# Kernel optimization log

Hardware: AMD Instinct MI355X
Metric: run time of the kernel (lower is better)

Reference implementation:

```python
import jax, jax.numpy as jnp
import numpy as np

B, S, D_MODEL = 4, 4096, 1024
H, KD, F = 16, 64, 256
KERNEL_SCALE = 1.0
NORM = 1.0 / np.sqrt(KD).astype(np.float32)  # 1/sqrt(key_dim)
EPS = 1e-6


def setup_inputs() -> dict:
    key = jax.random.key(0)
    ks = jax.random.split(key, 12)
    s = 0.02
    x = jax.random.normal(ks[0], (B, S, D_MODEL), dtype=jnp.float32)
    Wq = jax.random.normal(ks[1], (D_MODEL, H * KD), dtype=jnp.float32) * s
    bq = jnp.zeros((H * KD,), jnp.float32)
    Wk = jax.random.normal(ks[2], (D_MODEL, H * KD), dtype=jnp.float32) * s
    bk = jnp.zeros((H * KD,), jnp.float32)
    Wv = jax.random.normal(ks[3], (D_MODEL, H * KD), dtype=jnp.float32) * s
    bv = jnp.zeros((H * KD,), jnp.float32)
    # RFF params (non-trainable in original; orthogonal-ish random here)
    rff_W = jax.random.normal(ks[4], (KD, F), dtype=jnp.float32)
    q_, _ = jnp.linalg.qr(rff_W.T)  # (F, KD) -> orthonormal rows subset
    rff_W = q_.T[:KD, :F].astype(jnp.float32)
    rff_b = jax.random.uniform(ks[5], (F,), jnp.float32, 0.0, 2.0 * np.pi)
    Wo = jax.random.normal(ks[6], (H * KD, D_MODEL), dtype=jnp.float32) * s
    bo = jnp.zeros((D_MODEL,), jnp.float32)
    return {"x": x, "Wq": Wq, "bq": bq, "Wk": Wk, "bk": bk, "Wv": Wv,
            "bv": bv, "rff_W": rff_W, "rff_b": rff_b, "Wo": Wo, "bo": bo}


def _split_heads(t):
    # [B, S, H*KD] -> [B, H, S, KD]
    return t.reshape(B, S, H, KD).transpose(0, 2, 1, 3)


def _rff(t, rff_W, rff_b):
    # RandomFourierFeatures: cos((x*scale) @ W + b) * sqrt(2/F)
    proj = jnp.einsum('bhsd,df->bhsf', t * KERNEL_SCALE, rff_W) + rff_b
    return jnp.cos(proj) * np.sqrt(2.0 / F).astype(np.float32)


def reference(x, Wq, bq, Wk, bk, Wv, bv, rff_W, rff_b, Wo, bo):
    q = _split_heads(x @ Wq + bq)  # [B,H,S,KD]
    k = _split_heads(x @ Wk + bk)
    v = _split_heads(x @ Wv + bv)
    q_prime = _rff(q * NORM, rff_W, rff_b)  # [B,H,S,F]
    k_prime = _rff(k * NORM, rff_W, rff_b)
    # Non-causal FAVOR+ linear attention: O(L)
    kv = jnp.einsum('bhsf,bhsd->bhfd', k_prime, v)          # [B,H,F,KD]
    k_sum = jnp.sum(k_prime, axis=2)                         # [B,H,F]
    num = jnp.einsum('bhsf,bhfd->bhsd', q_prime, kv)         # [B,H,S,KD]
    den = jnp.einsum('bhsf,bhf->bhs', q_prime, k_sum)        # [B,H,S]
    out = num / (den + EPS)[..., None]
    out = out.transpose(0, 2, 1, 3).reshape(B, S, H * KD)    # merge heads
    return out @ Wo + bo
```

## Files before the change

kernel.cpp:

```cpp
#include <hip/hip_runtime.h>
#include <hip/hip_bf16.h>
#include <math.h>

#define B_SZ    4
#define S_LEN   4096
#define DMODEL  1024
#define NH      16
#define KDIM    64
#define NF      256
#define NROWS   (B_SZ * S_LEN)
#define NCHUNK  8
#define RFF_SCALE 0.08838834764831845f
#define NORM_Q    0.125f

typedef __attribute__((ext_vector_type(8))) short s8v;
typedef __attribute__((ext_vector_type(4))) float f4v;

static __device__ __forceinline__ unsigned short f2bf(float f) {
  unsigned u = __float_as_uint(f);
  unsigned r = (u + 0x7FFFu + ((u >> 16) & 1u)) >> 16;
  return (unsigned short)r;
}

#define MFMA16(a, b, c) __builtin_amdgcn_mfma_f32_16x16x32_bf16((a), (b), (c), 0, 0, 0)

__device__ __forceinline__ void glds16(const void* g, void* l) {
  __builtin_amdgcn_global_load_lds(
      (const __attribute__((address_space(1))) void*)g,
      (__attribute__((address_space(3))) void*)l, 16, 0, 0);
}

__global__ __launch_bounds__(256) void cast_bf16_kernel(
    const float* __restrict__ src, unsigned short* __restrict__ dst, int n8)
{
  int i = blockIdx.x * 256 + threadIdx.x;
  if (i >= n8) return;
  const float* s = src + (size_t)i * 8;
  float4 a = *(const float4*)s;
  float4 b = *(const float4*)(s + 4);
  union { s8v v; unsigned short u[8]; } o;
  o.u[0]=f2bf(a.x); o.u[1]=f2bf(a.y); o.u[2]=f2bf(a.z); o.u[3]=f2bf(a.w);
  o.u[4]=f2bf(b.x); o.u[5]=f2bf(b.y); o.u[6]=f2bf(b.z); o.u[7]=f2bf(b.w);
  *(s8v*)(dst + (size_t)i * 8) = o.v;
}

__global__ __launch_bounds__(256) void transpose_cast_kernel(
    const float* __restrict__ W, unsigned short* __restrict__ WT)
{
  __shared__ float t[32][33];
  const int k0 = blockIdx.y * 32, n0 = blockIdx.x * 32;
  const int c = threadIdx.x & 31, r4 = threadIdx.x >> 5;
#pragma unroll
  for (int i = 0; i < 4; ++i) {
    int row = r4 + i * 8;
    t[row][c] = W[(size_t)(k0 + row) * 1024 + n0 + c];
  }
  __syncthreads();
#pragma unroll
  for (int i = 0; i < 4; ++i) {
    int row = r4 + i * 8;
    WT[(size_t)(n0 + row) * 1024 + k0 + c] = f2bf(t[c][row]);
  }
}

__global__ __launch_bounds__(256) void prep_rff_kernel(
    const float* __restrict__ rffW, unsigned short* __restrict__ rffWT)
{
  int i = blockIdx.x * 256 + threadIdx.x;
  int f = i >> 6, d = i & 63;
  rffWT[(size_t)f * 64 + d] = f2bf(rffW[(size_t)d * 256 + f] * NORM_Q);
}

template <int OUT_BF16, int QKV_FUSED>
__global__ __launch_bounds__(512, 2) void gemm_bt_kernel(
    const unsigned short* __restrict__ A,
    const unsigned short* __restrict__ BT0,
    const unsigned short* __restrict__ BT1,
    const unsigned short* __restrict__ BT2,
    const float* __restrict__ bias0, const float* __restrict__ bias1,
    const float* __restrict__ bias2,
    void* __restrict__ out0, void* __restrict__ out1, void* __restrict__ out2,
    int M, int N, int K, int NXT)
{
  __shared__ __align__(16) unsigned short As[2][16384];
  __shared__ __align__(16) unsigned short Bs[2][16384];
  const int tid = threadIdx.x;
  const int lane = tid & 63, wave = tid >> 6;

  int wg = blockIdx.x;
  {
    const int nwg = gridDim.x;
    const int q = nwg >> 3, r = nwg & 7;
    const int xcd = wg & 7, pos = wg >> 3;
    wg = (xcd < r ? xcd * (q + 1) : r * (q + 1) + (xcd - r) * q) + pos;
  }
  const int m0 = (wg / NXT) * 256;
  int ngl = (wg % NXT) * 256;
  const unsigned short* BT = BT0;
  const float* bias = bias0;
  void* outp = out0;
  if (QKV_FUSED) {
    int which = ngl >> 10;
    if (which == 1) { BT = BT1; bias = bias1; outp = out1; }
    else if (which == 2) { BT = BT2; bias = bias2; outp = out2; }
    ngl &= 1023;
  }
  const int n0 = ngl;

  const int trow = tid >> 3;
  const int g8 = (((lane & 7) ^ (trow & 7)) * 8);
  const unsigned short* aPtr = A  + (size_t)(m0 + trow) * K + g8;
  const unsigned short* bPtr = BT + (size_t)(n0 + trow) * K + g8;
  const int NT = K >> 6;

  auto STAGE = [&](int ts, int h) {
    if (ts >= NT) return;
    const int buf = ts & 1, half = h >> 1;
    const size_t go = (size_t)half * 128 * K + (size_t)ts * 64;
    if ((h & 1) == 0) {
      unsigned short* lp = &As[buf][half * 8192 + wave * 512];
      glds16(aPtr + go, lp);
      glds16(aPtr + go + (size_t)64 * K, lp + 4096);
    } else {
      unsigned short* lp = &Bs[buf][half * 8192 + wave * 512];
      glds16(bPtr + go, lp);
      glds16(bPtr + go + (size_t)64 * K, lp + 4096);
    }
  };

  const int col = lane & 15, quad = lane >> 4;
  const int wm = (wave >> 2) * 128;
  const int wn = (wave & 3) * 64;
  const int c7 = col & 7;
  const int idxA0 = (wm + col) * 64 + ((quad ^ c7) * 8);
  const int idxA1 = (wm + col) * 64 + (((4 + quad) ^ c7) * 8);
  const int idxB0 = (wn + col) * 64 + ((quad ^ c7) * 8);
  const int idxB1 = (wn + col) * 64 + (((4 + quad) ^ c7) * 8);

  f4v acc[2][4][4];
  const f4v zz = {0.f, 0.f, 0.f, 0.f};
#pragma unroll
  for (int h = 0; h < 2; ++h)
#pragma unroll
    for (int i = 0; i < 4; ++i)
#pragma unroll
      for (int j = 0; j < 4; ++j) acc[h][i][j] = zz;

  STAGE(0, 0); STAGE(0, 1); STAGE(0, 2); STAGE(0, 3);
  STAGE(1, 0); STAGE(1, 1); STAGE(1, 2);
  asm volatile("s_waitcnt vmcnt(6)" ::: "memory");
  __builtin_amdgcn_s_barrier();

  s8v a0[4][2], a1[4][2], b0[2][2], b1[2][2];
  {
    const unsigned short* pA = As[0];
    const unsigned short* pB = Bs[0];
#pragma unroll
    for (int u = 0; u < 2; ++u) {
      b0[u][0] = *(const s8v*)&pB[idxB0 + u * 1024];
      b0[u][1] = *(const s8v*)&pB[idxB1 + u * 1024];
    }
#pragma unroll
    for (int x = 0; x < 4; ++x) {
      a0[x][0] = *(const s8v*)&pA[idxA0 + x * 1024];
      a0[x][1] = *(const s8v*)&pA[idxA1 + x * 1024];
    }
  }

  for (int t = 0; t < NT; ++t) {
    const int buf = t & 1;
    const unsigned short* pA = As[buf];
    const unsigned short* pB = Bs[buf];
    const unsigned short* qA = As[buf ^ 1];
    const unsigned short* qB = Bs[buf ^ 1];

    __builtin_amdgcn_s_barrier();
    asm volatile("s_waitcnt lgkmcnt(0)" ::: "memory");
    __builtin_amdgcn_sched_barrier(0);
#pragma unroll
    for (int u = 0; u < 2; ++u) {
      b1[u][0] = *(const s8v*)&pB[idxB0 + 2048 + u * 1024];
      b1[u][1] = *(const s8v*)&pB[idxB1 + 2048 + u * 1024];
    }
    __builtin_amdgcn_sched_barrier(0);
#pragma unroll
    for (int x = 0; x < 4; ++x) {
      a1[x][0] = *(const s8v*)&pA[idxA0 + 4096 + x * 1024];
      a1[x][1] = *(const s8v*)&pA[idxA1 + 4096 + x * 1024];
    }
    __builtin_amdgcn_sched_barrier(0);
    __builtin_amdgcn_s_setprio(1);
#pragma unroll
    for (int x = 0; x < 4; ++x)
#pragma unroll
      for (int u = 0; u < 2; ++u) {
        acc[0][x][u] = MFMA16(a0[x][0], b0[u][0], acc[0][x][u]);
        acc[0][x][u] = MFMA16(a0[x][1], b0[u][1], acc[0][x][u]);
      }
    __builtin_amdgcn_s_setprio(0);
    __builtin_amdgcn_sched_barrier(0);

    __builtin_amdgcn_s_barrier();
    STAGE(t + 1, 3);
    asm volatile("s_waitcnt lgkmcnt(8)" ::: "memory");
    __builtin_amdgcn_sched_barrier(0);
    __builtin_amdgcn_s_setprio(1);
#pragma unroll
    for (int x = 0; x < 4; ++x)
#pragma unroll
      for (int u = 0; u < 2; ++u) {
        acc[0][x][2 + u] = MFMA16(a0[x][0], b1[u][0], acc[0][x][2 + u]);
        acc[0][x][2 + u] = MFMA16(a0[x][1], b1[u][1], acc[0][x][2 + u]);
      }
    __builtin_amdgcn_s_setprio(0);
    __builtin_amdgcn_sched_barrier(0);

    __builtin_amdgcn_s_barrier();
    STAGE(t + 2, 1);
    asm volatile("s_waitcnt lgkmcnt(0)" ::: "memory");
    __builtin_amdgcn_sched_barrier(0);
    __builtin_amdgcn_s_setprio(1);
#pragma unroll
    for (int x = 0; x < 4; ++x)
#pragma unroll
      for (int u = 0; u < 2; ++u) {
        acc[1][x][2 + u] = MFMA16(a1[x][0], b1[u][0], acc[1][x][2 + u]);
        acc[1][x][2 + u] = MFMA16(a1[x][1], b1[u][1], acc[1][x][2 + u]);
      }
    __builtin_amdgcn_s_setprio(0);
    __builtin_amdgcn_sched_barrier(0);

    __builtin_amdgcn_s_barrier();
    STAGE(t + 2, 0);
    STAGE(t + 2, 2);
    if (t < NT - 2) asm volatile("s_waitcnt vmcnt(6)" ::: "memory");
    else            asm volatile("s_waitcnt vmcnt(0)" ::: "memory");
    __builtin_amdgcn_sched_barrier(0);
    s8v b0n[2][2], a0n[4][2];
#pragma unroll
    for (int u = 0; u < 2; ++u) {
      b0n[u][0] = *(const s8v*)&qB[idxB0 + u * 1024];
      b0n[u][1] = *(const s8v*)&qB[idxB1 + u * 1024];
    }
    __builtin_amdgcn_sched_barrier(0);
#pragma unroll
    for (int x = 0; x < 4; ++x) {
      a0n[x][0] = *(const s8v*)&qA[idxA0 + x * 1024];
      a0n[x][1] = *(const s8v*)&qA[idxA1 + x * 1024];
    }
    __builtin_amdgcn_sched_barrier(0);
    __builtin_amdgcn_s_setprio(1);
#pragma unroll
    for (int x = 0; x < 4; ++x)
#pragma unroll
      for (int u = 0; u < 2; ++u) {
        acc[1][x][u] = MFMA16(a1[x][0], b0[u][0], acc[1][x][u]);
        acc[1][x][u] = MFMA16(a1[x][1], b0[u][1], acc[1][x][u]);
      }
    __builtin_amdgcn_s_setprio(0);
    __builtin_amdgcn_sched_barrier(0);
#pragma unroll
    for (int u = 0; u < 2; ++u) { b0[u][0] = b0n[u][0]; b0[u][1] = b0n[u][1]; }
#pragma unroll
    for (int x = 0; x < 4; ++x) { a0[x][0] = a0n[x][0]; a0[x][1] = a0n[x][1]; }
  }

#pragma unroll
  for (int h = 0; h < 2; ++h) {
#pragma unroll
    for (int i = 0; i < 4; ++i) {
#pragma unroll
      for (int j = 0; j < 4; ++j) {
        int n = n0 + wn + j * 16 + col;
        float bv = bias[n];
#pragma unroll
        for (int r = 0; r < 4; ++r) {
          int m = m0 + wm + h * 64 + i * 16 + quad * 4 + r;
          float v = acc[h][i][j][r] + bv;
          if (OUT_BF16)
            ((unsigned short*)outp)[(size_t)m * N + n] = f2bf(v);
          else
            ((float*)outp)[(size_t)m * N + n] = v;
        }
      }
    }
  }
}

__global__ __launch_bounds__(256) void kv_kernel(
    const unsigned short* __restrict__ kg, const unsigned short* __restrict__ vg,
    const unsigned short* __restrict__ rffWT, const float* __restrict__ rffb,
    float* __restrict__ pkv)
{
  __shared__ __align__(16) unsigned short vT[80 * 72];
  __shared__ __align__(16) unsigned short kps[256 * 72];
  const int bh = blockIdx.x, chunk = blockIdx.y;
  const int b = bh >> 4, h = bh & 15;
  const int tid = threadIdx.x;
  const int lane = tid & 63, wave = tid >> 6;
  const int col = lane & 15, quad = lane >> 4;
  const f4v zz = {0.f, 0.f, 0.f, 0.f};

  s8v wf[2][4];
  float bfv[4];
#pragma unroll
  for (int ks = 0; ks < 2; ++ks)
#pragma unroll
    for (int t = 0; t < 4; ++t)
      wf[ks][t] = *(const s8v*)(rffWT +
          (size_t)(wave * 64 + t * 16 + col) * 64 + ks * 32 + quad * 8);
#pragma unroll
  for (int j = 0; j < 4; ++j) bfv[j] = rffb[wave * 64 + j * 16 + col];

  for (int e = tid; e < 1024; e += 256) {
    int r = 64 + (e >> 6), s = e & 63;
    vT[r * 72 + s] = (r == 64) ? (unsigned short)0x3F80 : (unsigned short)0;
  }

  f4v kvacc[4][5];
#pragma unroll
  for (int i = 0; i < 4; ++i)
#pragma unroll
    for (int j = 0; j < 5; ++j) kvacc[i][j] = zz;

  const int sA = tid & 63,        chA = tid >> 6;
  const int sB = (tid + 256) & 63, chB = (tid + 256) >> 6;

  union U { s8v v; unsigned short u[8]; };
  U v0, v1;
  s8v kf[2][4];
  {
    const int s0 = chunk * 512;
    v0.v = *(const s8v*)(vg + ((size_t)(b * S_LEN + s0 + sA)) * DMODEL + h * KDIM + chA * 8);
    v1.v = *(const s8v*)(vg + ((size_t)(b * S_LEN + s0 + sB)) * DMODEL + h * KDIM + chB * 8);
#pragma unroll
    for (int ks = 0; ks < 2; ++ks)
#pragma unroll
      for (int t = 0; t < 4; ++t)
        kf[ks][t] = *(const s8v*)(kg +
            ((size_t)(b * S_LEN + s0 + t * 16 + col)) * DMODEL + h * KDIM + ks * 32 + quad * 8);
  }

  for (int st = 0; st < 8; ++st) {
    const int s0 = chunk * 512 + st * 64;
    __syncthreads();
#pragma unroll
    for (int j = 0; j < 8; ++j) vT[(chA * 8 + j) * 72 + sA] = v0.u[j];
#pragma unroll
    for (int j = 0; j < 8; ++j) vT[(chB * 8 + j) * 72 + sB] = v1.u[j];
    f4v p[4][4];
#pragma unroll
    for (int i = 0; i < 4; ++i)
#pragma unroll
      for (int j = 0; j < 4; ++j) p[i][j] = zz;
#pragma unroll
    for (int ks = 0; ks < 2; ++ks)
#pragma unroll
      for (int i = 0; i < 4; ++i)
#pragma unroll
        for (int j = 0; j < 4; ++j) p[i][j] = MFMA16(kf[ks][i], wf[ks][j], p[i][j]);
    U n0, n1;
    s8v kn[2][4];
    if (st < 7) {
      const int s1 = s0 + 64;
      n0.v = *(const s8v*)(vg + ((size_t)(b * S_LEN + s1 + sA)) * DMODEL + h * KDIM + chA * 8);
      n1.v = *(const s8v*)(vg + ((size_t)(b * S_LEN + s1 + sB)) * DMODEL + h * KDIM + chB * 8);
#pragma unroll
      for (int ks = 0; ks < 2; ++ks)
#pragma unroll
        for (int t = 0; t < 4; ++t)
          kn[ks][t] = *(const s8v*)(kg +
              ((size_t)(b * S_LEN + s1 + t * 16 + col)) * DMODEL + h * KDIM + ks * 32 + quad * 8);
    }
#pragma unroll
    for (int j = 0; j < 4; ++j) {
      int f = wave * 64 + j * 16 + col;
#pragma unroll
      for (int i = 0; i < 4; ++i) {
        union { unsigned long long d; unsigned short u[4]; } pk;
#pragma unroll
        for (int r = 0; r < 4; ++r)
          pk.u[r] = f2bf(__cosf(p[i][j][r] + bfv[j]) * RFF_SCALE);
        *(unsigned long long*)&kps[f * 72 + i * 16 + quad * 4] = pk.d;
      }
    }
    __syncthreads();
#pragma unroll
    for (int ks = 0; ks < 2; ++ks) {
      s8v af[4], bf[5];
#pragma unroll
      for (int t = 0; t < 4; ++t)
        af[t] = *(const s8v*)&kps[(wave * 64 + t * 16 + col) * 72 + ks * 32 + quad * 8];
#pragma unroll
      for (int t = 0; t < 5; ++t)
        bf[t] = *(const s8v*)&vT[(t * 16 + col) * 72 + ks * 32 + quad * 8];
#pragma unroll
      for (int i = 0; i < 4; ++i)
#pragma unroll
        for (int j = 0; j < 5; ++j)
          kvacc[i][j] = MFMA16(af[i], bf[j], kvacc[i][j]);
    }
    v0 = n0; v1 = n1;
#pragma unroll
    for (int ks = 0; ks < 2; ++ks)
#pragma unroll
      for (int t = 0; t < 4; ++t) kf[ks][t] = kn[ks][t];
  }
  const size_t base = ((size_t)(chunk * 64 + bh)) * NF * 80;
#pragma unroll
  for (int i = 0; i < 4; ++i)
#pragma unroll
    for (int r = 0; r < 4; ++r) {
      int f = wave * 64 + i * 16 + quad * 4 + r;
#pragma unroll
      for (int j = 0; j < 5; ++j)
        pkv[base + (size_t)f * 80 + j * 16 + col] = kvacc[i][j][r];
    }
}

__global__ __launch_bounds__(256) void reduce_kv_kernel(
    const float* __restrict__ pkv, unsigned short* __restrict__ kvT)
{
  __shared__ unsigned short lt[80 * 64];
  const int bh = blockIdx.x >> 2, qt = blockIdx.x & 3;
  const int f0 = qt * 64;
  for (int e = threadIdx.x; e < 64 * 80; e += 256) {
    int fl = e / 80, d = e - fl * 80;
    float s = 0.f;
#pragma unroll
    for (int c = 0; c < NCHUNK; ++c)
      s += pkv[((size_t)(c * 64 + bh)) * NF * 80 + (size_t)(f0 + fl) * 80 + d];
    lt[d * 64 + fl] = f2bf(s);
  }
  __syncthreads();
  for (int o = threadIdx.x; o < 80 * 64; o += 256) {
    int d = o >> 6, fl = o & 63;
    kvT[(size_t)bh * 80 * NF + d * 256 + f0 + fl] = lt[o];
  }
}

__global__ __launch_bounds__(256) void attn_kernel(
    const unsigned short* __restrict__ qg, const unsigned short* __restrict__ kvTg,
    const unsigned short* __restrict__ rffWT, const float* __restrict__ rffb,
    unsigned short* __restrict__ att)
{
  __shared__ __align__(16) unsigned short qps[64 * 264];
  __shared__ __align__(16) unsigned short kvs[80 * 264];
  const int bh = blockIdx.x;
  const int b = bh >> 4, h = bh & 15;
  const int tid = threadIdx.x;
  const int lane = tid & 63, wave = tid >> 6;
  const int col = lane & 15, quad = lane >> 4;
  const f4v zz = {0.f, 0.f, 0.f, 0.f};

  s8v wf[2][4];
  float bfv[4];
#pragma unroll
  for (int ks = 0; ks < 2; ++ks)
#pragma unroll
    for (int t = 0; t < 4; ++t)
      wf[ks][t] = *(const s8v*)(rffWT +
          (size_t)(wave * 64 + t * 16 + col) * 64 + ks * 32 + quad * 8);
#pragma unroll
  for (int j = 0; j < 4; ++j) bfv[j] = rffb[wave * 64 + j * 16 + col];

  for (int c = tid; c < 2560; c += 256) {
    int d = c >> 5, ch = c & 31;
    *(s8v*)&kvs[d * 264 + ch * 8] =
        *(const s8v*)(kvTg + (size_t)bh * 80 * NF + d * 256 + ch * 8);
  }

  s8v qf[2][4];
  {
    const int s0 = blockIdx.y * 512;
#pragma unroll
    for (int ks = 0; ks < 2; ++ks)
#pragma unroll
      for (int t = 0; t < 4; ++t)
        qf[ks][t] = *(const s8v*)(qg +
            ((size_t)(b * S_LEN + s0 + t * 16 + col)) * DMODEL + h * KDIM + ks * 32 + quad * 8);
  }

  for (int it = 0; it < 8; ++it) {
    const int s0 = blockIdx.y * 512 + it * 64;
    f4v p[4][4];
#pragma unroll
    for (int i = 0; i < 4; ++i)
#pragma unroll
      for (int j = 0; j < 4; ++j) p[i][j] = zz;
#pragma unroll
    for (int ks = 0; ks < 2; ++ks)
#pragma unroll
      for (int i = 0; i < 4; ++i)
#pragma unroll
        for (int j = 0; j < 4; ++j) p[i][j] = MFMA16(qf[ks][i], wf[ks][j], p[i][j]);
    s8v qn[2][4];
    if (it < 7) {
      const int s1 = s0 + 64;
#pragma unroll
      for (int ks = 0; ks < 2; ++ks)
#pragma unroll
        for (int t = 0; t < 4; ++t)
          qn[ks][t] = *(const s8v*)(qg +
              ((size_t)(b * S_LEN + s1 + t * 16 + col)) * DMODEL + h * KDIM + ks * 32 + quad * 8);
    }
    __syncthreads();
#pragma unroll
    for (int j = 0; j < 4; ++j) {
      int f = wave * 64 + j * 16 + col;
#pragma unroll
      for (int i = 0; i < 4; ++i)
#pragma unroll
        for (int r = 0; r < 4; ++r) {
          int s = i * 16 + quad * 4 + r;
          qps[s * 264 + f] = f2bf(__cosf(p[i][j][r] + bfv[j]) * RFF_SCALE);
        }
    }
    __syncthreads();
    f4v acc[5];
#pragma unroll
    for (int j = 0; j < 5; ++j) acc[j] = zz;
#pragma unroll
    for (int k0 = 0; k0 < 256; k0 += 32) {
      s8v af = *(const s8v*)&qps[(wave * 16 + col) * 264 + k0 + quad * 8];
      s8v bf[5];
#pragma unroll
      for (int t = 0; t < 5; ++t)
        bf[t] = *(const s8v*)&kvs[(t * 16 + col) * 264 + k0 + quad * 8];
#pragma unroll
      for (int j = 0; j < 5; ++j) acc[j] = MFMA16(af, bf[j], acc[j]);
    }
    float inv[4];
#pragma unroll
    for (int r = 0; r < 4; ++r) {
      float den = __shfl(acc[4][r], lane & 48);
      inv[r] = 1.0f / (den + 1e-6f);
    }
#pragma unroll
    for (int r = 0; r < 4; ++r) {
      int m = s0 + wave * 16 + quad * 4 + r;
      size_t obase = ((size_t)(b * S_LEN + m)) * DMODEL + h * KDIM;
#pragma unroll
      for (int j = 0; j < 4; ++j)
        att[obase + j * 16 + col] = f2bf(acc[j][r] * inv[r]);
    }
#pragma unroll
    for (int ks = 0; ks < 2; ++ks)
#pragma unroll
      for (int t = 0; t < 4; ++t) qf[ks][t] = qn[ks][t];
  }
}

extern "C" void kernel_launch(void* const* d_in, const int* in_sizes, int n_in,
                              void* d_out, int out_size, void* d_ws, size_t ws_size,
                              hipStream_t stream)
{
  const float* x    = (const float*)d_in[0];
  const float* Wq   = (const float*)d_in[1];
  const float* bq   = (const float*)d_in[2];
  const float* Wk   = (const float*)d_in[3];
  const float* bk   = (const float*)d_in[4];
  const float* Wv   = (const float*)d_in[5];
  const float* bv   = (const float*)d_in[6];
  const float* rffW = (const float*)d_in[7];
  const float* rffb = (const float*)d_in[8];
  const float* Wo   = (const float*)d_in[9];
  const float* bo   = (const float*)d_in[10];
  float* out = (float*)d_out;

  char* w = (char*)d_ws;
  const size_t XB = (size_t)NROWS * DMODEL * 2;
  const size_t WT = (size_t)DMODEL * DMODEL * 2;
  unsigned short* xb   = (unsigned short*)(w);
  unsigned short* WqT  = (unsigned short*)(w + XB);
  unsigned short* WkT  = (unsigned short*)(w + XB + WT);
  unsigned short* WvT  = (unsigned short*)(w + XB + 2 * WT);
  unsigned short* WoT  = (unsigned short*)(w + XB + 3 * WT);
  unsigned short* rWT  = (unsigned short*)(w + XB + 4 * WT);
  char* p = w + XB + 4 * WT + 65536;
  unsigned short* qb = (unsigned short*)(p);
  unsigned short* kb = (unsigned short*)(p + XB);
  unsigned short* vb = (unsigned short*)(p + 2 * XB);
  float* pkv         = (float*)(p + 3 * XB);
  unsigned short* kvT = (unsigned short*)(p + 3 * XB + (size_t)NCHUNK * 64 * NF * 80 * 4);
  unsigned short* att = kb;

  cast_bf16_kernel<<<NROWS * DMODEL / 8 / 256, 256, 0, stream>>>(x, xb, NROWS * DMODEL / 8);
  dim3 tg(32, 32);
  transpose_cast_kernel<<<tg, 256, 0, stream>>>(Wq, WqT);
  transpose_cast_kernel<<<tg, 256, 0, stream>>>(Wk, WkT);
  transpose_cast_kernel<<<tg, 256, 0, stream>>>(Wv, WvT);
  transpose_cast_kernel<<<tg, 256, 0, stream>>>(Wo, WoT);
  prep_rff_kernel<<<64, 256, 0, stream>>>(rffW, rWT);

  gemm_bt_kernel<1, 1><<<768, 512, 0, stream>>>(
      xb, WqT, WkT, WvT, bq, bk, bv, qb, kb, vb, NROWS, DMODEL, DMODEL, 12);

  kv_kernel<<<dim3(64, NCHUNK), 256, 0, stream>>>(kb, vb, rWT, rffb, pkv);
  reduce_kv_kernel<<<256, 256, 0, stream>>>(pkv, kvT);
  attn_kernel<<<dim3(64, 8), 256, 0, stream>>>(qb, kvT, rWT, rffb, att);

  gemm_bt_kernel<0, 0><<<256, 512, 0, stream>>>(
      att, WoT, nullptr, nullptr, bo, nullptr, nullptr, out, nullptr, nullptr,
      NROWS, DMODEL, DMODEL, 4);
}
```

Before: 404.1 us.

## Restructure GEMM LDS pipeline, compute k_sum in registers, split RFF MFMA phases

The GEMM main loop is reorganised so each quarter loads its fragments from LDS right before use, issues one global STAGE, then synchronises. This replaces the earlier cross-iteration register prefetch of the next tile's a0/b0 fragments, which should lower register pressure but adds more barriers. The kv kernel drops the padded ones-row trick for k_sum and accumulates it in registers with a shuffle reduction, removing one MFMA column block of work and LDS space. The RFF projections in the kv and q kernels are split into two halves so the cosine work on one half can overlap the MFMAs of the other, and the reduce kernel skips the unused padding columns.

```diff
diff --git a/kernel.cpp b/kernel.cpp
--- a/kernel.cpp
+++ b/kernel.cpp
@@ -147,62 +147,88 @@
       for (int j = 0; j < 4; ++j) acc[h][i][j] = zz;
 
   STAGE(0, 0); STAGE(0, 1); STAGE(0, 2); STAGE(0, 3);
+  asm volatile("s_waitcnt vmcnt(4)" ::: "memory");
   STAGE(1, 0); STAGE(1, 1); STAGE(1, 2);
   asm volatile("s_waitcnt vmcnt(6)" ::: "memory");
   __builtin_amdgcn_s_barrier();
-
-  s8v a0[4][2], a1[4][2], b0[2][2], b1[2][2];
-  {
-    const unsigned short* pA = As[0];
-    const unsigned short* pB = Bs[0];
-#pragma unroll
-    for (int u = 0; u < 2; ++u) {
-      b0[u][0] = *(const s8v*)&pB[idxB0 + u * 1024];
-      b0[u][1] = *(const s8v*)&pB[idxB1 + u * 1024];
-    }
-#pragma unroll
-    for (int x = 0; x < 4; ++x) {
-      a0[x][0] = *(const s8v*)&pA[idxA0 + x * 1024];
-      a0[x][1] = *(const s8v*)&pA[idxA1 + x * 1024];
-    }
-  }
 
   for (int t = 0; t < NT; ++t) {
     const int buf = t & 1;
     const unsigned short* pA = As[buf];
     const unsigned short* pB = Bs[buf];
-    const unsigned short* qA = As[buf ^ 1];
-    const unsigned short* qB = Bs[buf ^ 1];
-
+    s8v a0[4][2], a1[4][2], b0[2][2], b1[2][2];
+
+#pragma unroll
+    for (int x = 0; x < 4; ++x) {
+      a0[x][0] = *(const s8v*)&pA[idxA0 + x * 1024];
+      a0[x][1] = *(const s8v*)&pA[idxA1 + x * 1024];
+    }
+#pragma unroll
+    for (int u = 0; u < 2; ++u) {
+      b0[u][0] = *(const s8v*)&pB[idxB0 + u * 1024];
+      b0[u][1] = *(const s8v*)&pB[idxB1 + u * 1024];
+    }
+    STAGE(t + 1, 3);
     __builtin_amdgcn_s_barrier();
     asm volatile("s_waitcnt lgkmcnt(0)" ::: "memory");
     __builtin_amdgcn_sched_barrier(0);
+    __builtin_amdgcn_s_setprio(1);
+#pragma unroll
+    for (int x = 0; x < 4; ++x)
+#pragma unroll
+      for (int u = 0; u < 2; ++u) {
+        acc[0][x][u] = MFMA16(a0[x][0], b0[u][0], acc[0][x][u]);
+        acc[0][x][u] = MFMA16(a0[x][1], b0[u][1], acc[0][x][u]);
+      }
+    __builtin_amdgcn_s_setprio(0);
+    __builtin_amdgcn_sched_barrier(0);
+    __builtin_amdgcn_s_barrier();
+
+#pragma unroll
+    for (int x = 0; x < 4; ++x) {
+      a1[x][0] = *(const s8v*)&pA[idxA0 + 4096 + x * 1024];
+      a1[x][1] = *(const s8v*)&pA[idxA1 + 4096 + x * 1024];
+    }
+    STAGE(t + 2, 0);
+    __builtin_amdgcn_s_barrier();
+    asm volatile("s_waitcnt lgkmcnt(0)" ::: "memory");
+    __builtin_amdgcn_sched_barrier(0);
+    __builtin_amdgcn_s_setprio(1);
+#pragma unroll
+    for (int x = 0; x < 4; ++x)
+#pragma unroll
+      for (int u = 0; u < 2; ++u) {
+        acc[1][x][u] = MFMA16(a1[x][0], b0[u][0], acc[1][x][u]);
+        acc[1][x][u] = MFMA16(a1[x][1], b0[u][1], acc[1][x][u]);
+      }
+    __builtin_amdgcn_s_setprio(0);
+    __builtin_amdgcn_sched_barrier(0);
+    __builtin_amdgcn_s_barrier();
+
 #pragma unroll
     for (int u = 0; u < 2; ++u) {
       b1[u][0] = *(const s8v*)&pB[idxB0 + 2048 + u * 1024];
       b1[u][1] = *(const s8v*)&pB[idxB1 + 2048 + u * 1024];
     }
-    __builtin_amdgcn_sched_barrier(0);
-#pragma unroll
-    for (int x = 0; x < 4; ++x) {
-      a1[x][0] = *(const s8v*)&pA[idxA0 + 4096 + x * 1024];
-      a1[x][1] = *(const s8v*)&pA[idxA1 + 4096 + x * 1024];
-    }
+    STAGE(t + 2, 1);
+    __builtin_amdgcn_s_barrier();
+    asm volatile("s_waitcnt lgkmcnt(0)" ::: "memory");
     __builtin_amdgcn_sched_barrier(0);
     __builtin_amdgcn_s_setprio(1);
 #pragma unroll
     for (int x = 0; x < 4; ++x)
 #pragma unroll
       for (int u = 0; u < 2; ++u) {
-        acc[0][x][u] = MFMA16(a0[x][0], b0[u][0], acc[0][x][u]);
-        acc[0][x][u] = MFMA16(a0[x][1], b0[u][1], acc[0][x][u]);
+        acc[1][x][2 + u] = MFMA16(a1[x][0], b1[u][0], acc[1][x][2 + u]);
+        acc[1][x][2 + u] = MFMA16(a1[x][1], b1[u][1], acc[1][x][2 + u]);
       }
     __builtin_amdgcn_s_setprio(0);
     __builtin_amdgcn_sched_barrier(0);
-
-    __builtin_amdgcn_s_barrier();
-    STAGE(t + 1, 3);
-    asm volatile("s_waitcnt lgkmcnt(8)" ::: "memory");
+    __builtin_amdgcn_s_barrier();
+
+    STAGE(t + 2, 2);
+    __builtin_amdgcn_s_barrier();
+    asm volatile("s_waitcnt lgkmcnt(0)" ::: "memory");
     __builtin_amdgcn_sched_barrier(0);
     __builtin_amdgcn_s_setprio(1);
 #pragma unroll
@@ -214,55 +240,9 @@
       }
     __builtin_amdgcn_s_setprio(0);
     __builtin_amdgcn_sched_barrier(0);
-
-    __builtin_amdgcn_s_barrier();
-    STAGE(t + 2, 1);
-    asm volatile("s_waitcnt lgkmcnt(0)" ::: "memory");
-    __builtin_amdgcn_sched_barrier(0);
-    __builtin_amdgcn_s_setprio(1);
-#pragma unroll
-    for (int x = 0; x < 4; ++x)
-#pragma unroll
-      for (int u = 0; u < 2; ++u) {
-        acc[1][x][2 + u] = MFMA16(a1[x][0], b1[u][0], acc[1][x][2 + u]);
-        acc[1][x][2 + u] = MFMA16(a1[x][1], b1[u][1], acc[1][x][2 + u]);
-      }
-    __builtin_amdgcn_s_setprio(0);
-    __builtin_amdgcn_sched_barrier(0);
-
-    __builtin_amdgcn_s_barrier();
-    STAGE(t + 2, 0);
-    STAGE(t + 2, 2);
     if (t < NT - 2) asm volatile("s_waitcnt vmcnt(6)" ::: "memory");
     else            asm volatile("s_waitcnt vmcnt(0)" ::: "memory");
-    __builtin_amdgcn_sched_barrier(0);
-    s8v b0n[2][2], a0n[4][2];
-#pragma unroll
-    for (int u = 0; u < 2; ++u) {
-      b0n[u][0] = *(const s8v*)&qB[idxB0 + u * 1024];
-      b0n[u][1] = *(const s8v*)&qB[idxB1 + u * 1024];
-    }
-    __builtin_amdgcn_sched_barrier(0);
-#pragma unroll
-    for (int x = 0; x < 4; ++x) {
-      a0n[x][0] = *(const s8v*)&qA[idxA0 + x * 1024];
-      a0n[x][1] = *(const s8v*)&qA[idxA1 + x * 1024];
-    }
-    __builtin_amdgcn_sched_barrier(0);
-    __builtin_amdgcn_s_setprio(1);
-#pragma unroll
-    for (int x = 0; x < 4; ++x)
-#pragma unroll
-      for (int u = 0; u < 2; ++u) {
-        acc[1][x][u] = MFMA16(a1[x][0], b0[u][0], acc[1][x][u]);
-        acc[1][x][u] = MFMA16(a1[x][1], b0[u][1], acc[1][x][u]);
-      }
-    __builtin_amdgcn_s_setprio(0);
-    __builtin_amdgcn_sched_barrier(0);
-#pragma unroll
-    for (int u = 0; u < 2; ++u) { b0[u][0] = b0n[u][0]; b0[u][1] = b0n[u][1]; }
-#pragma unroll
-    for (int x = 0; x < 4; ++x) { a0[x][0] = a0n[x][0]; a0[x][1] = a0n[x][1]; }
+    __builtin_amdgcn_s_barrier();
   }
 
 #pragma unroll
@@ -292,7 +272,7 @@
     const unsigned short* __restrict__ rffWT, const float* __restrict__ rffb,
     float* __restrict__ pkv)
 {
-  __shared__ __align__(16) unsigned short vT[80 * 72];
+  __shared__ __align__(16) unsigned short vT[64 * 72];
   __shared__ __align__(16) unsigned short kps[256 * 72];
   const int bh = blockIdx.x, chunk = blockIdx.y;
   const int b = bh >> 4, h = bh & 15;
@@ -312,18 +292,14 @@
 #pragma unroll
   for (int j = 0; j < 4; ++j) bfv[j] = rffb[wave * 64 + j * 16 + col];
 
-  for (int e = tid; e < 1024; e += 256) {
-    int r = 64 + (e >> 6), s = e & 63;
-    vT[r * 72 + s] = (r == 64) ? (unsigned short)0x3F80 : (unsigned short)0;
-  }
-
-  f4v kvacc[4][5];
+  f4v kvacc[4][4];
 #pragma unroll
   for (int i = 0; i < 4; ++i)
 #pragma unroll
-    for (int j = 0; j < 5; ++j) kvacc[i][j] = zz;
-
-  const int sA = tid & 63,        chA = tid >> 6;
+    for (int j = 0; j < 4; ++j) kvacc[i][j] = zz;
+  float ksum[4] = {0.f, 0.f, 0.f, 0.f};
+
+  const int sA = tid & 63,         chA = tid >> 6;
   const int sB = (tid + 256) & 63, chB = (tid + 256) >> 6;
 
   union U { s8v v; unsigned short u[8]; };
@@ -348,17 +324,20 @@
     for (int j = 0; j < 8; ++j) vT[(chA * 8 + j) * 72 + sA] = v0.u[j];
 #pragma unroll
     for (int j = 0; j < 8; ++j) vT[(chB * 8 + j) * 72 + sB] = v1.u[j];
-    f4v p[4][4];
-#pragma unroll
-    for (int i = 0; i < 4; ++i)
-#pragma unroll
-      for (int j = 0; j < 4; ++j) p[i][j] = zz;
+
+    f4v p01[2][4];
+#pragma unroll
+    for (int i = 0; i < 2; ++i)
+#pragma unroll
+      for (int j = 0; j < 4; ++j) p01[i][j] = zz;
 #pragma unroll
     for (int ks = 0; ks < 2; ++ks)
 #pragma unroll
-      for (int i = 0; i < 4; ++i)
-#pragma unroll
-        for (int j = 0; j < 4; ++j) p[i][j] = MFMA16(kf[ks][i], wf[ks][j], p[i][j]);
+      for (int i = 0; i < 2; ++i)
+#pragma unroll
+        for (int j = 0; j < 4; ++j)
+          p01[i][j] = MFMA16(kf[ks][i], wf[ks][j], p01[i][j]);
+
     U n0, n1;
     s8v kn[2][4];
     if (st < 7) {
@@ -372,50 +351,96 @@
           kn[ks][t] = *(const s8v*)(kg +
               ((size_t)(b * S_LEN + s1 + t * 16 + col)) * DMODEL + h * KDIM + ks * 32 + quad * 8);
     }
+
+#pragma unroll
+    for (int i = 0; i < 2; ++i)
+#pragma unroll
+      for (int j = 0; j < 4; ++j) {
+        int f = wave * 64 + j * 16 + col;
+        union { unsigned long long d; unsigned short u[4]; } pk;
+#pragma unroll
+        for (int r = 0; r < 4; ++r) {
+          float cv = __cosf(p01[i][j][r] + bfv[j]) * RFF_SCALE;
+          ksum[j] += cv;
+          pk.u[r] = f2bf(cv);
+        }
+        *(unsigned long long*)&kps[f * 72 + i * 16 + quad * 4] = pk.d;
+      }
+
+    f4v p23[2][4];
+#pragma unroll
+    for (int i = 0; i < 2; ++i)
+#pragma unroll
+      for (int j = 0; j < 4; ++j) p23[i][j] = zz;
+#pragma unroll
+    for (int ks = 0; ks < 2; ++ks)
+#pragma unroll
+      for (int i = 0; i < 2; ++i)
+#pragma unroll
+        for (int j = 0; j < 4; ++j)
+          p23[i][j] = MFMA16(kf[ks][2 + i], wf[ks][j], p23[i][j]);
+#pragma unroll
+    for (int i = 0; i < 2; ++i)
+#pragma unroll
+      for (int j = 0; j < 4; ++j) {
+        int f = wave * 64 + j * 16 + col;
+        union { unsigned long long d; unsigned short u[4]; } pk;
+#pragma unroll
+        for (int r = 0; r < 4; ++r) {
+          float cv = __cosf(p23[i][j][r] + bfv[j]) * RFF_SCALE;
+          ksum[j] += cv;
+          pk.u[r] = f2bf(cv);
+        }
+        *(unsigned long long*)&kps[f * 72 + (2 + i) * 16 + quad * 4] = pk.d;
+      }
+    __syncthreads();
+
+#pragma unroll
+    for (int ks = 0; ks < 2; ++ks) {
+      s8v af[4], bf[4];
+#pragma unroll
+      for (int t = 0; t < 4; ++t)
+        af[t] = *(const s8v*)&kps[(wave * 64 + t * 16 + col) * 72 + ks * 32 + quad * 8];
+#pragma unroll
+      for (int t = 0; t < 4; ++t)
+        bf[t] = *(const s8v*)&vT[(t * 16 + col) * 72 + ks * 32 + quad * 8];
+#pragma unroll
+      for (int i = 0; i < 4; ++i)
+#pragma unroll
+        for (int j = 0; j < 4; ++j)
+          kvacc[i][j] = MFMA16(af[i], bf[j], kvacc[i][j]);
+    }
+    if (st < 7) {
+      v0 = n0; v1 = n1;
+#pragma unroll
+      for (int ks = 0; ks < 2; ++ks)
+#pragma unroll
+        for (int t = 0; t < 4; ++t) kf[ks][t] = kn[ks][t];
+    }
+  }
+
+  const size_t base = ((size_t)(chunk * 64 + bh)) * NF * 80;
+#pragma unroll
+  for (int i = 0; i < 4; ++i)
+#pragma unroll
+    for (int r = 0; r < 4; ++r) {
+      int f = wave * 64 + i * 16 + quad * 4 + r;
+#pragma unroll
+      for (int j = 0; j < 4; ++j)
+        pkv[base + (size_t)f * 80 + j * 16 + col] = kvacc[i][j][r];
+    }
+#pragma unroll
+  for (int j = 0; j < 4; ++j) {
+    ksum[j] += __shfl_xor(ksum[j], 16);
+    ksum[j] += __shfl_xor(ksum[j], 32);
+  }
+  if (quad == 0) {
 #pragma unroll
     for (int j = 0; j < 4; ++j) {
       int f = wave * 64 + j * 16 + col;
-#pragma unroll
-      for (int i = 0; i < 4; ++i) {
-        union { unsigned long long d; unsigned short u[4]; } pk;
-#pragma unroll
-        for (int r = 0; r < 4; ++r)
-          pk.u[r] = f2bf(__cosf(p[i][j][r] + bfv[j]) * RFF_SCALE);
-        *(unsigned long long*)&kps[f * 72 + i * 16 + quad * 4] = pk.d;
-      }
-    }
-    __syncthreads();
-#pragma unroll
-    for (int ks = 0; ks < 2; ++ks) {
-      s8v af[4], bf[5];
-#pragma unroll
-      for (int t = 0; t < 4; ++t)
-        af[t] = *(const s8v*)&kps[(wave * 64 + t * 16 + col) * 72 + ks * 32 + quad * 8];
-#pragma unroll
-      for (int t = 0; t < 5; ++t)
-        bf[t] = *(const s8v*)&vT[(t * 16 + col) * 72 + ks * 32 + quad * 8];
-#pragma unroll
-      for (int i = 0; i < 4; ++i)
-#pragma unroll
-        for (int j = 0; j < 5; ++j)
-          kvacc[i][j] = MFMA16(af[i], bf[j], kvacc[i][j]);
-    }
-    v0 = n0; v1 = n1;
-#pragma unroll
-    for (int ks = 0; ks < 2; ++ks)
-#pragma unroll
-      for (int t = 0; t < 4; ++t) kf[ks][t] = kn[ks][t];
-  }
-  const size_t base = ((size_t)(chunk * 64 + bh)) * NF * 80;
-#pragma unroll
-  for (int i = 0; i < 4; ++i)
-#pragma unroll
-    for (int r = 0; r < 4; ++r) {
-      int f = wave * 64 + i * 16 + quad * 4 + r;
-#pragma unroll
-      for (int j = 0; j < 5; ++j)
-        pkv[base + (size_t)f * 80 + j * 16 + col] = kvacc[i][j][r];
-    }
+      pkv[base + (size_t)f * 80 + 64] = ksum[j];
+    }
+  }
 }
 
 __global__ __launch_bounds__(256) void reduce_kv_kernel(
@@ -427,9 +452,11 @@
   for (int e = threadIdx.x; e < 64 * 80; e += 256) {
     int fl = e / 80, d = e - fl * 80;
     float s = 0.f;
-#pragma unroll
-    for (int c = 0; c < NCHUNK; ++c)
-      s += pkv[((size_t)(c * 64 + bh)) * NF * 80 + (size_t)(f0 + fl) * 80 + d];
+    if (d <= 64) {
+#pragma unroll
+      for (int c = 0; c < NCHUNK; ++c)
+        s += pkv[((size_t)(c * 64 + bh)) * NF * 80 + (size_t)(f0 + fl) * 80 + d];
+    }
     lt[d * 64 + fl] = f2bf(s);
   }
   __syncthreads();
@@ -483,17 +510,18 @@
 
   for (int it = 0; it < 8; ++it) {
     const int s0 = blockIdx.y * 512 + it * 64;
-    f4v p[4][4];
-#pragma unroll
-    for (int i = 0; i < 4; ++i)
-#pragma unroll
-      for (int j = 0; j < 4; ++j) p[i][j] = zz;
+    f4v p01[2][4];
+#pragma unroll
+    for (int i = 0; i < 2; ++i)
+#pragma unroll
+      for (int j = 0; j < 4; ++j) p01[i][j] = zz;
 #pragma unroll
     for (int ks = 0; ks < 2; ++ks)
 #pragma unroll
-      for (int i = 0; i < 4; ++i)
-#pragma unroll
-        for (int j = 0; j < 4; ++j) p[i][j] = MFMA16(qf[ks][i], wf[ks][j], p[i][j]);
+      for (int i = 0; i < 2; ++i)
+#pragma unroll
+        for (int j = 0; j < 4; ++j)
+          p01[i][j] = MFMA16(qf[ks][i], wf[ks][j], p01[i][j]);
     s8v qn[2][4];
     if (it < 7) {
       const int s1 = s0 + 64;
@@ -506,16 +534,39 @@
     }
     __syncthreads();
 #pragma unroll
-    for (int j = 0; j < 4; ++j) {
-      int f = wave * 64 + j * 16 + col;
-#pragma unroll
-      for (int i = 0; i < 4; ++i)
+    for (int i = 0; i < 2; ++i)
+#pragma unroll
+      for (int j = 0; j < 4; ++j) {
+        int f = wave * 64 + j * 16 + col;
 #pragma unroll
         for (int r = 0; r < 4; ++r) {
           int s = i * 16 + quad * 4 + r;
-          qps[s * 264 + f] = f2bf(__cosf(p[i][j][r] + bfv[j]) * RFF_SCALE);
+          qps[s * 264 + f] = f2bf(__cosf(p01[i][j][r] + bfv[j]) * RFF_SCALE);
         }
-    }
+      }
+    f4v p23[2][4];
+#pragma unroll
+    for (int i = 0; i < 2; ++i)
+#pragma unroll
+      for (int j = 0; j < 4; ++j) p23[i][j] = zz;
+#pragma unroll
+    for (int ks = 0; ks < 2; ++ks)
+#pragma unroll
+      for (int i = 0; i < 2; ++i)
+#pragma unroll
+        for (int j = 0; j < 4; ++j)
+          p23[i][j] = MFMA16(qf[ks][2 + i], wf[ks][j], p23[i][j]);
+#pragma unroll
+    for (int i = 0; i < 2; ++i)
+#pragma unroll
+      for (int j = 0; j < 4; ++j) {
+        int f = wave * 64 + j * 16 + col;
+#pragma unroll
+        for (int r = 0; r < 4; ++r) {
+          int s = (2 + i) * 16 + quad * 4 + r;
+          qps[s * 264 + f] = f2bf(__cosf(p23[i][j][r] + bfv[j]) * RFF_SCALE);
+        }
+      }
     __syncthreads();
     f4v acc[5];
 #pragma unroll
@@ -544,10 +595,12 @@
       for (int j = 0; j < 4; ++j)
         att[obase + j * 16 + col] = f2bf(acc[j][r] * inv[r]);
     }
-#pragma unroll
-    for (int ks = 0; ks < 2; ++ks)
-#pragma unroll
-      for (int t = 0; t < 4; ++t) qf[ks][t] = qn[ks][t];
+    if (it < 7) {
+#pragma unroll
+      for (int ks = 0; ks < 2; ++ks)
+#pragma unroll
+        for (int t = 0; t < 4; ++t) qf[ks][t] = qn[ks][t];
+    }
   }
 }
 
```

Result: no change. 409.3 us (+1.3%).

## Restructure GEMM main loop schedule and XOR-swizzle LDS layouts in attention kernels

Applied to the files above, without the earlier changes.

Rewrites the GEMM inner loop so each iteration loads its own A/B fragments from LDS instead of prefetching the next tile's fragments into registers, and reorders STAGE issues and barriers across four MFMA phases. The kv, attention-apply and reduce kernels replace padded LDS row strides (72/264) with XOR-swizzled unpadded layouts, and the reduce kernel pads its transpose buffer. The aim is fewer LDS bank conflicts, lower LDS footprint and lower register pressure. The cost is more barriers and less overlap of LDS reads with MFMA in the GEMM, and the extra vmcnt(4) wait in the prologue may stall.

```diff
diff --git a/kernel.cpp b/kernel.cpp
--- a/kernel.cpp
+++ b/kernel.cpp
@@ -147,47 +147,30 @@
       for (int j = 0; j < 4; ++j) acc[h][i][j] = zz;
 
   STAGE(0, 0); STAGE(0, 1); STAGE(0, 2); STAGE(0, 3);
+  asm volatile("s_waitcnt vmcnt(4)" ::: "memory");
   STAGE(1, 0); STAGE(1, 1); STAGE(1, 2);
   asm volatile("s_waitcnt vmcnt(6)" ::: "memory");
   __builtin_amdgcn_s_barrier();
-
-  s8v a0[4][2], a1[4][2], b0[2][2], b1[2][2];
-  {
-    const unsigned short* pA = As[0];
-    const unsigned short* pB = Bs[0];
-#pragma unroll
-    for (int u = 0; u < 2; ++u) {
-      b0[u][0] = *(const s8v*)&pB[idxB0 + u * 1024];
-      b0[u][1] = *(const s8v*)&pB[idxB1 + u * 1024];
-    }
-#pragma unroll
-    for (int x = 0; x < 4; ++x) {
-      a0[x][0] = *(const s8v*)&pA[idxA0 + x * 1024];
-      a0[x][1] = *(const s8v*)&pA[idxA1 + x * 1024];
-    }
-  }
 
   for (int t = 0; t < NT; ++t) {
     const int buf = t & 1;
     const unsigned short* pA = As[buf];
     const unsigned short* pB = Bs[buf];
-    const unsigned short* qA = As[buf ^ 1];
-    const unsigned short* qB = Bs[buf ^ 1];
-
+    s8v a0[4][2], a1[4][2], b0[2][2], b1[2][2];
+
+#pragma unroll
+    for (int x = 0; x < 4; ++x) {
+      a0[x][0] = *(const s8v*)&pA[idxA0 + x * 1024];
+      a0[x][1] = *(const s8v*)&pA[idxA1 + x * 1024];
+    }
+#pragma unroll
+    for (int u = 0; u < 2; ++u) {
+      b0[u][0] = *(const s8v*)&pB[idxB0 + u * 1024];
+      b0[u][1] = *(const s8v*)&pB[idxB1 + u * 1024];
+    }
+    STAGE(t + 1, 3);
     __builtin_amdgcn_s_barrier();
     asm volatile("s_waitcnt lgkmcnt(0)" ::: "memory");
-    __builtin_amdgcn_sched_barrier(0);
-#pragma unroll
-    for (int u = 0; u < 2; ++u) {
-      b1[u][0] = *(const s8v*)&pB[idxB0 + 2048 + u * 1024];
-      b1[u][1] = *(const s8v*)&pB[idxB1 + 2048 + u * 1024];
-    }
-    __builtin_amdgcn_sched_barrier(0);
-#pragma unroll
-    for (int x = 0; x < 4; ++x) {
-      a1[x][0] = *(const s8v*)&pA[idxA0 + 4096 + x * 1024];
-      a1[x][1] = *(const s8v*)&pA[idxA1 + 4096 + x * 1024];
-    }
     __builtin_amdgcn_sched_barrier(0);
     __builtin_amdgcn_s_setprio(1);
 #pragma unroll
@@ -199,10 +182,53 @@
       }
     __builtin_amdgcn_s_setprio(0);
     __builtin_amdgcn_sched_barrier(0);
-
-    __builtin_amdgcn_s_barrier();
-    STAGE(t + 1, 3);
-    asm volatile("s_waitcnt lgkmcnt(8)" ::: "memory");
+    __builtin_amdgcn_s_barrier();
+
+#pragma unroll
+    for (int x = 0; x < 4; ++x) {
+      a1[x][0] = *(const s8v*)&pA[idxA0 + 4096 + x * 1024];
+      a1[x][1] = *(const s8v*)&pA[idxA1 + 4096 + x * 1024];
+    }
+    STAGE(t + 2, 0);
+    __builtin_amdgcn_s_barrier();
+    asm volatile("s_waitcnt lgkmcnt(0)" ::: "memory");
+    __builtin_amdgcn_sched_barrier(0);
+    __builtin_amdgcn_s_setprio(1);
+#pragma unroll
+    for (int x = 0; x < 4; ++x)
+#pragma unroll
+      for (int u = 0; u < 2; ++u) {
+        acc[1][x][u] = MFMA16(a1[x][0], b0[u][0], acc[1][x][u]);
+        acc[1][x][u] = MFMA16(a1[x][1], b0[u][1], acc[1][x][u]);
+      }
+    __builtin_amdgcn_s_setprio(0);
+    __builtin_amdgcn_sched_barrier(0);
+    __builtin_amdgcn_s_barrier();
+
+#pragma unroll
+    for (int u = 0; u < 2; ++u) {
+      b1[u][0] = *(const s8v*)&pB[idxB0 + 2048 + u * 1024];
+      b1[u][1] = *(const s8v*)&pB[idxB1 + 2048 + u * 1024];
+    }
+    STAGE(t + 2, 1);
+    __builtin_amdgcn_s_barrier();
+    asm volatile("s_waitcnt lgkmcnt(0)" ::: "memory");
+    __builtin_amdgcn_sched_barrier(0);
+    __builtin_amdgcn_s_setprio(1);
+#pragma unroll
+    for (int x = 0; x < 4; ++x)
+#pragma unroll
+      for (int u = 0; u < 2; ++u) {
+        acc[1][x][2 + u] = MFMA16(a1[x][0], b1[u][0], acc[1][x][2 + u]);
+        acc[1][x][2 + u] = MFMA16(a1[x][1], b1[u][1], acc[1][x][2 + u]);
+      }
+    __builtin_amdgcn_s_setprio(0);
+    __builtin_amdgcn_sched_barrier(0);
+    __builtin_amdgcn_s_barrier();
+
+    STAGE(t + 2, 2);
+    __builtin_amdgcn_s_barrier();
+    asm volatile("s_waitcnt lgkmcnt(0)" ::: "memory");
     __builtin_amdgcn_sched_barrier(0);
     __builtin_amdgcn_s_setprio(1);
 #pragma unroll
@@ -214,55 +240,9 @@
       }
     __builtin_amdgcn_s_setprio(0);
     __builtin_amdgcn_sched_barrier(0);
-
-    __builtin_amdgcn_s_barrier();
-    STAGE(t + 2, 1);
-    asm volatile("s_waitcnt lgkmcnt(0)" ::: "memory");
-    __builtin_amdgcn_sched_barrier(0);
-    __builtin_amdgcn_s_setprio(1);
-#pragma unroll
-    for (int x = 0; x < 4; ++x)
-#pragma unroll
-      for (int u = 0; u < 2; ++u) {
-        acc[1][x][2 + u] = MFMA16(a1[x][0], b1[u][0], acc[1][x][2 + u]);
-        acc[1][x][2 + u] = MFMA16(a1[x][1], b1[u][1], acc[1][x][2 + u]);
-      }
-    __builtin_amdgcn_s_setprio(0);
-    __builtin_amdgcn_sched_barrier(0);
-
-    __builtin_amdgcn_s_barrier();
-    STAGE(t + 2, 0);
-    STAGE(t + 2, 2);
     if (t < NT - 2) asm volatile("s_waitcnt vmcnt(6)" ::: "memory");
     else            asm volatile("s_waitcnt vmcnt(0)" ::: "memory");
-    __builtin_amdgcn_sched_barrier(0);
-    s8v b0n[2][2], a0n[4][2];
-#pragma unroll
-    for (int u = 0; u < 2; ++u) {
-      b0n[u][0] = *(const s8v*)&qB[idxB0 + u * 1024];
-      b0n[u][1] = *(const s8v*)&qB[idxB1 + u * 1024];
-    }
-    __builtin_amdgcn_sched_barrier(0);
-#pragma unroll
-    for (int x = 0; x < 4; ++x) {
-      a0n[x][0] = *(const s8v*)&qA[idxA0 + x * 1024];
-      a0n[x][1] = *(const s8v*)&qA[idxA1 + x * 1024];
-    }
-    __builtin_amdgcn_sched_barrier(0);
-    __builtin_amdgcn_s_setprio(1);
-#pragma unroll
-    for (int x = 0; x < 4; ++x)
-#pragma unroll
-      for (int u = 0; u < 2; ++u) {
-        acc[1][x][u] = MFMA16(a1[x][0], b0[u][0], acc[1][x][u]);
-        acc[1][x][u] = MFMA16(a1[x][1], b0[u][1], acc[1][x][u]);
-      }
-    __builtin_amdgcn_s_setprio(0);
-    __builtin_amdgcn_sched_barrier(0);
-#pragma unroll
-    for (int u = 0; u < 2; ++u) { b0[u][0] = b0n[u][0]; b0[u][1] = b0n[u][1]; }
-#pragma unroll
-    for (int x = 0; x < 4; ++x) { a0[x][0] = a0n[x][0]; a0[x][1] = a0n[x][1]; }
+    __builtin_amdgcn_s_barrier();
   }
 
 #pragma unroll
@@ -292,13 +272,14 @@
     const unsigned short* __restrict__ rffWT, const float* __restrict__ rffb,
     float* __restrict__ pkv)
 {
-  __shared__ __align__(16) unsigned short vT[80 * 72];
-  __shared__ __align__(16) unsigned short kps[256 * 72];
+  __shared__ __align__(16) unsigned short vT[80 * 64];
+  __shared__ __align__(16) unsigned short kps[256 * 64];
   const int bh = blockIdx.x, chunk = blockIdx.y;
   const int b = bh >> 4, h = bh & 15;
   const int tid = threadIdx.x;
   const int lane = tid & 63, wave = tid >> 6;
   const int col = lane & 15, quad = lane >> 4;
+  const int c7 = col & 7;
   const f4v zz = {0.f, 0.f, 0.f, 0.f};
 
   s8v wf[2][4];
@@ -314,7 +295,8 @@
 
   for (int e = tid; e < 1024; e += 256) {
     int r = 64 + (e >> 6), s = e & 63;
-    vT[r * 72 + s] = (r == 64) ? (unsigned short)0x3F80 : (unsigned short)0;
+    vT[r * 64 + (((s >> 3) ^ (r & 7)) * 8) + (s & 7)] =
+        (r == 64) ? (unsigned short)0x3F80 : (unsigned short)0;
   }
 
   f4v kvacc[4][5];
@@ -323,7 +305,7 @@
 #pragma unroll
     for (int j = 0; j < 5; ++j) kvacc[i][j] = zz;
 
-  const int sA = tid & 63,        chA = tid >> 6;
+  const int sA = tid & 63,         chA = tid >> 6;
   const int sB = (tid + 256) & 63, chB = (tid + 256) >> 6;
 
   union U { s8v v; unsigned short u[8]; };
@@ -345,9 +327,11 @@
     const int s0 = chunk * 512 + st * 64;
     __syncthreads();
 #pragma unroll
-    for (int j = 0; j < 8; ++j) vT[(chA * 8 + j) * 72 + sA] = v0.u[j];
-#pragma unroll
-    for (int j = 0; j < 8; ++j) vT[(chB * 8 + j) * 72 + sB] = v1.u[j];
+    for (int j = 0; j < 8; ++j)
+      vT[(chA * 8 + j) * 64 + (((sA >> 3) ^ j) * 8) + (sA & 7)] = v0.u[j];
+#pragma unroll
+    for (int j = 0; j < 8; ++j)
+      vT[(chB * 8 + j) * 64 + (((sB >> 3) ^ j) * 8) + (sB & 7)] = v1.u[j];
     f4v p[4][4];
 #pragma unroll
     for (int i = 0; i < 4; ++i)
@@ -381,7 +365,8 @@
 #pragma unroll
         for (int r = 0; r < 4; ++r)
           pk.u[r] = f2bf(__cosf(p[i][j][r] + bfv[j]) * RFF_SCALE);
-        *(unsigned long long*)&kps[f * 72 + i * 16 + quad * 4] = pk.d;
+        int sc = i * 2 + (quad >> 1);
+        *(unsigned long long*)&kps[f * 64 + ((sc ^ c7) * 8) + (quad & 1) * 4] = pk.d;
       }
     }
     __syncthreads();
@@ -390,21 +375,25 @@
       s8v af[4], bf[5];
 #pragma unroll
       for (int t = 0; t < 4; ++t)
-        af[t] = *(const s8v*)&kps[(wave * 64 + t * 16 + col) * 72 + ks * 32 + quad * 8];
+        af[t] = *(const s8v*)&kps[(wave * 64 + t * 16 + col) * 64 +
+                                  (((ks * 4 + quad) ^ c7) * 8)];
 #pragma unroll
       for (int t = 0; t < 5; ++t)
-        bf[t] = *(const s8v*)&vT[(t * 16 + col) * 72 + ks * 32 + quad * 8];
+        bf[t] = *(const s8v*)&vT[(t * 16 + col) * 64 +
+                                 (((ks * 4 + quad) ^ c7) * 8)];
 #pragma unroll
       for (int i = 0; i < 4; ++i)
 #pragma unroll
         for (int j = 0; j < 5; ++j)
           kvacc[i][j] = MFMA16(af[i], bf[j], kvacc[i][j]);
     }
-    v0 = n0; v1 = n1;
-#pragma unroll
-    for (int ks = 0; ks < 2; ++ks)
-#pragma unroll
-      for (int t = 0; t < 4; ++t) kf[ks][t] = kn[ks][t];
+    if (st < 7) {
+      v0 = n0; v1 = n1;
+#pragma unroll
+      for (int ks = 0; ks < 2; ++ks)
+#pragma unroll
+        for (int t = 0; t < 4; ++t) kf[ks][t] = kn[ks][t];
+    }
   }
   const size_t base = ((size_t)(chunk * 64 + bh)) * NF * 80;
 #pragma unroll
@@ -421,7 +410,7 @@
 __global__ __launch_bounds__(256) void reduce_kv_kernel(
     const float* __restrict__ pkv, unsigned short* __restrict__ kvT)
 {
-  __shared__ unsigned short lt[80 * 64];
+  __shared__ unsigned short lt[80 * 66];
   const int bh = blockIdx.x >> 2, qt = blockIdx.x & 3;
   const int f0 = qt * 64;
   for (int e = threadIdx.x; e < 64 * 80; e += 256) {
@@ -430,12 +419,12 @@
 #pragma unroll
     for (int c = 0; c < NCHUNK; ++c)
       s += pkv[((size_t)(c * 64 + bh)) * NF * 80 + (size_t)(f0 + fl) * 80 + d];
-    lt[d * 64 + fl] = f2bf(s);
+    lt[d * 66 + fl] = f2bf(s);
   }
   __syncthreads();
   for (int o = threadIdx.x; o < 80 * 64; o += 256) {
     int d = o >> 6, fl = o & 63;
-    kvT[(size_t)bh * 80 * NF + d * 256 + f0 + fl] = lt[o];
+    kvT[(size_t)bh * 80 * NF + d * 256 + f0 + fl] = lt[d * 66 + fl];
   }
 }
 
@@ -444,13 +433,14 @@
     const unsigned short* __restrict__ rffWT, const float* __restrict__ rffb,
     unsigned short* __restrict__ att)
 {
-  __shared__ __align__(16) unsigned short qps[64 * 264];
-  __shared__ __align__(16) unsigned short kvs[80 * 264];
+  __shared__ __align__(16) unsigned short qps[64 * 256];
+  __shared__ __align__(16) unsigned short kvs[80 * 256];
   const int bh = blockIdx.x;
   const int b = bh >> 4, h = bh & 15;
   const int tid = threadIdx.x;
   const int lane = tid & 63, wave = tid >> 6;
   const int col = lane & 15, quad = lane >> 4;
+  const int c7 = col & 7;
   const f4v zz = {0.f, 0.f, 0.f, 0.f};
 
   s8v wf[2][4];
@@ -466,7 +456,7 @@
 
   for (int c = tid; c < 2560; c += 256) {
     int d = c >> 5, ch = c & 31;
-    *(s8v*)&kvs[d * 264 + ch * 8] =
+    *(s8v*)&kvs[d * 256 + ((ch ^ (d & 7)) * 8)] =
         *(const s8v*)(kvTg + (size_t)bh * 80 * NF + d * 256 + ch * 8);
   }
 
@@ -507,13 +497,15 @@
     __syncthreads();
 #pragma unroll
     for (int j = 0; j < 4; ++j) {
-      int f = wave * 64 + j * 16 + col;
+      int fc = wave * 8 + j * 2 + (col >> 3);
 #pragma unroll
       for (int i = 0; i < 4; ++i)
 #pragma unroll
         for (int r = 0; r < 4; ++r) {
           int s = i * 16 + quad * 4 + r;
-          qps[s * 264 + f] = f2bf(__cosf(p[i][j][r] + bfv[j]) * RFF_SCALE);
+          int s7 = (quad & 1) * 4 + r;
+          qps[s * 256 + ((fc ^ s7) * 8) + c7] =
+              f2bf(__cosf(p[i][j][r] + bfv[j]) * RFF_SCALE);
         }
     }
     __syncthreads();
@@ -522,11 +514,12 @@
     for (int j = 0; j < 5; ++j) acc[j] = zz;
 #pragma unroll
     for (int k0 = 0; k0 < 256; k0 += 32) {
-      s8v af = *(const s8v*)&qps[(wave * 16 + col) * 264 + k0 + quad * 8];
+      const int kc = k0 >> 3;
+      s8v af = *(const s8v*)&qps[(wave * 16 + col) * 256 + (((kc + quad) ^ c7) * 8)];
       s8v bf[5];
 #pragma unroll
       for (int t = 0; t < 5; ++t)
-        bf[t] = *(const s8v*)&kvs[(t * 16 + col) * 264 + k0 + quad * 8];
+        bf[t] = *(const s8v*)&kvs[(t * 16 + col) * 256 + (((kc + quad) ^ c7) * 8)];
 #pragma unroll
       for (int j = 0; j < 5; ++j) acc[j] = MFMA16(af, bf[j], acc[j]);
     }
@@ -544,10 +537,12 @@
       for (int j = 0; j < 4; ++j)
         att[obase + j * 16 + col] = f2bf(acc[j][r] * inv[r]);
     }
-#pragma unroll
-    for (int ks = 0; ks < 2; ++ks)
-#pragma unroll
-      for (int t = 0; t < 4; ++t) qf[ks][t] = qn[ks][t];
+    if (it < 7) {
+#pragma unroll
+      for (int ks = 0; ks < 2; ++ks)
+#pragma unroll
+        for (int t = 0; t < 4; ++t) qf[ks][t] = qn[ks][t];
+    }
   }
 }
 
```

New measurement: 415.2 us. 1.03x slower.
